# Optimization experiments

Measured on AMD Instinct MI355X. Metric: run time of the kernel, lower is better.

Reference implementation:

```python
import jax, jax.numpy as jnp
import numpy as np

HIDDEN = 2048
FFN = 8192
NUM_EXPERTS = 8
TOP_K = 2


def setup_inputs() -> dict:
    key = jax.random.key(0)
    ks = jax.random.split(key, 6)
    scale_h = 1.0 / np.sqrt(HIDDEN)
    scale_f = 1.0 / np.sqrt(FFN)
    return {
        "hidden_states": jax.random.normal(ks[0], (4, 2048, HIDDEN), jnp.float32),
        "gate_w": jax.random.normal(ks[1], (NUM_EXPERTS, HIDDEN), jnp.float32) * scale_h,
        "w1": jax.random.normal(ks[2], (NUM_EXPERTS, HIDDEN, FFN), jnp.float32) * scale_h,
        "b1": jax.random.normal(ks[3], (NUM_EXPERTS, FFN), jnp.float32) * 0.01,
        "w2": jax.random.normal(ks[4], (NUM_EXPERTS, FFN, HIDDEN), jnp.float32) * scale_f,
        "b2": jax.random.normal(ks[5], (NUM_EXPERTS, HIDDEN), jnp.float32) * 0.01,
    }


def reference(hidden_states, gate_w, w1, b1, w2, b2):
    B, S, H = hidden_states.shape
    E = gate_w.shape[0]
    tokens = hidden_states.reshape(-1, H)  # [T, H]

    # Router: softmax gate, top-2, renormalize selected weights
    logits = tokens @ gate_w.T  # [T, E]
    probs = jax.nn.softmax(logits, axis=-1)
    topk_w, topk_idx = jax.lax.top_k(probs, TOP_K)  # [T, 2]
    topk_w = topk_w / jnp.sum(topk_w, axis=-1, keepdims=True)

    # Dense combine weights: w_dense[t, e] = routing weight of token t for expert e
    w_dense = jnp.sum(jax.nn.one_hot(topk_idx, E, dtype=topk_w.dtype) * topk_w[..., None], axis=1)  # [T, E]

    # Per-expert FFN (exact GELU as nn.GELU default), weighted scatter-combine
    combined = jnp.zeros_like(tokens)
    for e in range(E):  # small fixed expert count
        h = jax.nn.gelu(tokens @ w1[e] + b1[e], approximate=False)  # [T, F]
        combined = combined + w_dense[:, e:e + 1] * (h @ w2[e] + b2[e])

    return combined.reshape(B, S, H) + hidden_states
```

## Files before the change

kernel.cpp:

```cpp
#include <hip/hip_runtime.h>
#include <hip/hip_bf16.h>

#define T_TOK 8192
#define HID 2048
#define FFN_ 8192
#define NE 8
#define MAXR 18432

typedef __attribute__((ext_vector_type(8))) short bf16x8;
typedef __attribute__((ext_vector_type(4))) float f32x4;
typedef __attribute__((ext_vector_type(8))) unsigned short u16x8;

__device__ __forceinline__ unsigned short f2bf(float f) {
  unsigned int u = __float_as_uint(f);
  u += 0x7fffu + ((u >> 16) & 1u);
  return (unsigned short)(u >> 16);
}
__device__ __forceinline__ float bf2f(unsigned short h) {
  return __uint_as_float(((unsigned int)h) << 16);
}

__device__ __forceinline__ void gload_lds16(const ushort* g, ushort* l) {
  __builtin_amdgcn_global_load_lds(
      (const __attribute__((address_space(1))) unsigned int*)g,
      (__attribute__((address_space(3))) unsigned int*)l, 16, 0, 0);
}

__device__ __forceinline__ float gelu_f(float v) {
  float u = v * (0.7978845608f + 0.0356774081f * v * v);
  float a = fabsf(u);
  float ex = __expf(-2.f * a);
  float r = 1.f / (1.f + ex);
  float th = (1.f - ex) * r;
  th = (u >= 0.f) ? th : -th;
  return 0.5f * v * (1.f + th);
}

__global__ __launch_bounds__(256) void router_kernel(
    const float* __restrict__ x, const float* __restrict__ gw,
    int* __restrict__ topk_idx, float* __restrict__ topk_w, int* __restrict__ counts)
{
  int lane = threadIdx.x & 63;
  int w = threadIdx.x >> 6;
  int t = blockIdx.x * 4 + w;
  const float* xr = x + (size_t)t * HID;
  float acc[NE];
#pragma unroll
  for (int e = 0; e < NE; ++e) acc[e] = 0.f;
  for (int h = lane; h < HID; h += 64) {
    float xv = xr[h];
#pragma unroll
    for (int e = 0; e < NE; ++e) acc[e] = fmaf(xv, gw[e * HID + h], acc[e]);
  }
#pragma unroll
  for (int e = 0; e < NE; ++e) {
#pragma unroll
    for (int s = 32; s > 0; s >>= 1) acc[e] += __shfl_xor(acc[e], s);
  }
  if (lane == 0) {
    int i0 = 0; float v0 = acc[0];
#pragma unroll
    for (int e = 1; e < NE; ++e) { if (acc[e] > v0) { v0 = acc[e]; i0 = e; } }
    int i1 = -1; float v1 = -3.4e38f;
#pragma unroll
    for (int e = 0; e < NE; ++e) { if (e != i0 && acc[e] > v1) { v1 = acc[e]; i1 = e; } }
    float r = __expf(v1 - v0);
    float w0 = 1.f / (1.f + r);
    float w1 = r * w0;
    topk_idx[2 * t] = i0; topk_idx[2 * t + 1] = i1;
    topk_w[2 * t] = w0;   topk_w[2 * t + 1] = w1;
    atomicAdd(&counts[i0], 1);
    atomicAdd(&counts[i1], 1);
  }
}

__global__ void offsets_kernel(const int* __restrict__ counts, int* __restrict__ offs) {
  if (threadIdx.x == 0 && blockIdx.x == 0) {
    int o = 0;
#pragma unroll
    for (int e = 0; e < NE; ++e) { offs[e] = o; o += (counts[e] + 255) & ~255; }
    offs[NE] = o;
  }
}

__global__ __launch_bounds__(256) void scatter_kernel(
    const int* __restrict__ topk_idx, const float* __restrict__ topk_w,
    const int* __restrict__ offs, int* __restrict__ cursors,
    int* __restrict__ slot_token, float* __restrict__ slot_w, int* __restrict__ token_slot)
{
  int t = blockIdx.x * blockDim.x + threadIdx.x;
  if (t >= T_TOK) return;
#pragma unroll
  for (int k = 0; k < 2; ++k) {
    int e = topk_idx[2 * t + k];
    int pos = atomicAdd(&cursors[e], 1);
    int slot = offs[e] + pos;
    slot_token[slot] = t;
    slot_w[slot] = topk_w[2 * t + k];
    token_slot[2 * t + k] = slot;
  }
}

__global__ __launch_bounds__(256) void gather_kernel(
    const float* __restrict__ x, const int* __restrict__ slot_token, ushort* __restrict__ Xg)
{
  int row = blockIdx.x;
  int tok = slot_token[row];
  ushort* dst = Xg + (size_t)row * HID + threadIdx.x * 8;
  if (tok < 0) {
    u16x8 z = {0, 0, 0, 0, 0, 0, 0, 0};
    *(u16x8*)dst = z;
  } else {
    const float* s = x + (size_t)tok * HID + threadIdx.x * 8;
    float4 a = *(const float4*)s;
    float4 b = *(const float4*)(s + 4);
    u16x8 v;
    v[0] = f2bf(a.x); v[1] = f2bf(a.y); v[2] = f2bf(a.z); v[3] = f2bf(a.w);
    v[4] = f2bf(b.x); v[5] = f2bf(b.y); v[6] = f2bf(b.z); v[7] = f2bf(b.w);
    *(u16x8*)dst = v;
  }
}

__global__ __launch_bounds__(256) void transpose_convert_kernel(
    const float* __restrict__ src, ushort* __restrict__ dst, int R, int C)
{
  __shared__ float tile[64][65];
  int e = blockIdx.z;
  const float* s = src + (size_t)e * R * C;
  ushort* d = dst + (size_t)e * R * C;
  int r0 = blockIdx.y << 6, c0 = blockIdx.x << 6;
  int t = threadIdx.x;
#pragma unroll
  for (int i = 0; i < 4; ++i) {
    int idx = i * 256 + t;
    int row = idx >> 4;
    int c4 = (idx & 15) << 2;
    float4 v = *(const float4*)&s[(size_t)(r0 + row) * C + (c0 + c4)];
    tile[row][c4 + 0] = v.x; tile[row][c4 + 1] = v.y;
    tile[row][c4 + 2] = v.z; tile[row][c4 + 3] = v.w;
  }
  __syncthreads();
#pragma unroll
  for (int i = 0; i < 8; ++i) {
    int idx = (i * 256 + t) * 2;
    int orow = idx >> 6;
    int ocol = idx & 63;
    ushort2 p;
    p.x = f2bf(tile[ocol][orow]);
    p.y = f2bf(tile[ocol + 1][orow]);
    *(ushort2*)&d[(size_t)(c0 + orow) * R + (r0 + ocol)] = p;
  }
}


#define WAIT_LGKM() do { asm volatile("s_waitcnt lgkmcnt(0)" ::: "memory"); \
                         __builtin_amdgcn_sched_barrier(0); } while (0)
#define WAIT_VM6()  do { asm volatile("s_waitcnt vmcnt(6)" ::: "memory");  \
                         __builtin_amdgcn_sched_barrier(0); } while (0)
#define WAIT_VM0()  do { asm volatile("s_waitcnt vmcnt(0)" ::: "memory");  \
                         __builtin_amdgcn_sched_barrier(0); } while (0)

#define STG_A(BUF, HALF, T) do {                                            \
    ushort* _d = lds + (BUF) * 32768 + (HALF) * 8192 + tid * 8;             \
    gload_lds16(sA0 + (size_t)(HALF) * 64 * K + (size_t)(T) * 64, _d);      \
    gload_lds16(sA1 + (size_t)(HALF) * 64 * K + (size_t)(T) * 64, _d + 4096); \
  } while (0)
#define STG_B(BUF, HALF, T) do {                                            \
    ushort* _d = lds + (BUF) * 32768 + 16384 + (HALF) * 8192 + tid * 8;     \
    gload_lds16(sB0 + (size_t)(HALF) * 32 * K + (size_t)(T) * 64, _d);      \
    gload_lds16(sB1 + (size_t)(HALF) * 32 * K + (size_t)(T) * 64, _d + 4096); \
  } while (0)

#define LDA(BUF, MQ) do {                                                   \
    _Pragma("unroll") for (int mm = 0; mm < 4; ++mm) {                      \
      const ushort* _p = lds + (BUF) * 32768 + (MQ) * 8192 + aoff + mm * 1024; \
      af[mm][0] = *(const bf16x8*)(_p + ck0);                               \
      af[mm][1] = *(const bf16x8*)(_p + ck1);                               \
    } } while (0)
#define LDB(BUF, NQ) do {                                                   \
    _Pragma("unroll") for (int nn = 0; nn < 2; ++nn) {                      \
      const ushort* _p = lds + (BUF) * 32768 + 16384 + (NQ) * 8192 + boff + nn * 1024; \
      bf[NQ][nn][0] = *(const bf16x8*)(_p + ck0);                           \
      bf[NQ][nn][1] = *(const bf16x8*)(_p + ck1);                           \
    } } while (0)

#define MFMA_Q(MQ, NQ) do {                                                 \
    _Pragma("unroll") for (int mm = 0; mm < 4; ++mm)                        \
    _Pragma("unroll") for (int nn = 0; nn < 2; ++nn) {                      \
      acc[(MQ)*4+mm][(NQ)*2+nn] = __builtin_amdgcn_mfma_f32_16x16x32_bf16(  \
          af[mm][0], bf[NQ][nn][0], acc[(MQ)*4+mm][(NQ)*2+nn], 0, 0, 0);    \
      acc[(MQ)*4+mm][(NQ)*2+nn] = __builtin_amdgcn_mfma_f32_16x16x32_bf16(  \
          af[mm][1], bf[NQ][nn][1], acc[(MQ)*4+mm][(NQ)*2+nn], 0, 0, 0);    \
    } } while (0)

#define PH_MFMA(MQ, NQ) do {                                                \
    __builtin_amdgcn_s_barrier();                                           \
    WAIT_LGKM();                                                            \
    __builtin_amdgcn_s_setprio(1);                                          \
    MFMA_Q(MQ, NQ);                                                         \
    __builtin_amdgcn_s_setprio(0);                                          \
    __builtin_amdgcn_sched_barrier(0);                                      \
  } while (0)

template <int EPI>
__global__ __launch_bounds__(512, 2) void gemm256_kernel(
    const ushort* __restrict__ A, const ushort* __restrict__ Bt,
    const float* __restrict__ bias, ushort* __restrict__ Cout,
    const float* __restrict__ slot_w, const int* __restrict__ offs,
    int K, int N, int gy)
{
  __shared__ ushort lds[65536];

  const int tid = threadIdx.x;
  int nwg = gridDim.x;
  int wg = blockIdx.x;
  int cpx = nwg >> 3;
  wg = (wg & 7) * cpx + (wg >> 3);
  int cb = wg / gy;
  int rb = wg - cb * gy;

  int total = offs[NE];
  int row0 = rb * 256;
  if (row0 >= total) return;
  int e = 0;
#pragma unroll
  for (int i = 1; i < NE; ++i) e += (row0 >= offs[i]) ? 1 : 0;

  const ushort* Ag = A + (size_t)row0 * K;
  const ushort* Bg = Bt + ((size_t)e * N + (size_t)cb * 256) * K;

  const int pr0 = tid >> 3;
  const int pr1 = 64 + pr0;
  const int j0 = (tid & 7) ^ (pr0 & 7);
  const int j1 = (tid & 7) ^ (pr1 & 7);
  const int rA0 = pr0;
  const int rA1 = 128 + pr0;
  const int rB0 = ((pr0 >> 5) << 6) + (pr0 & 31);
  const int rB1 = ((pr1 >> 5) << 6) + (pr1 & 31);
  const ushort* sA0 = Ag + (size_t)rA0 * K + j0 * 8;
  const ushort* sA1 = Ag + (size_t)rA1 * K + j1 * 8;
  const ushort* sB0 = Bg + (size_t)rB0 * K + j0 * 8;
  const ushort* sB1 = Bg + (size_t)rB1 * K + j1 * 8;

  const int lane = tid & 63;
  const int wid = tid >> 6;
  const int wr = wid >> 2, wc = wid & 3;
  const int lrow = lane & 15, g = lane >> 4, x7 = lrow & 7;
  const int ck0 = (g ^ x7) * 8;
  const int ck1 = ((4 + g) ^ x7) * 8;
  const int aoff = (wr * 64 + lrow) * 64;
  const int boff = (wc * 32 + lrow) * 64;

  f32x4 acc[8][4] = {};
  bf16x8 af[4][2], bf[2][2][2];

  const int NT = K >> 6;
  const int NITER = NT >> 1;

  STG_A(0, 0, 0); STG_A(0, 1, 0); STG_B(0, 0, 0); STG_B(0, 1, 0);
  STG_A(1, 0, 1); STG_B(1, 0, 1); STG_B(1, 1, 1);
  WAIT_VM6();
  __builtin_amdgcn_s_barrier();

  for (int it = 0; it < NITER; ++it) {
    const int tb = 2 * it + 1;
    const int tn0 = 2 * it + 2;
    const int tn1 = 2 * it + 3;
    const bool more0 = tn0 < NT;
    const bool more1 = tn1 < NT;

    LDA(0, 0); LDB(0, 0);
    STG_A(1, 1, tb);
    PH_MFMA(0, 0);
    __builtin_amdgcn_s_barrier();

    LDB(0, 1);
    if (more0) STG_A(0, 0, tn0);
    PH_MFMA(0, 1);
    __builtin_amdgcn_s_barrier();

    LDA(0, 1);
    if (more0) STG_B(0, 0, tn0);
    PH_MFMA(1, 0);
    __builtin_amdgcn_s_barrier();

    if (more0) STG_B(0, 1, tn0);
    PH_MFMA(1, 1);
    if (it + 1 < NITER) { WAIT_VM6(); } else { WAIT_VM0(); }
    __builtin_amdgcn_s_barrier();

    LDA(1, 0); LDB(1, 0);
    if (more0) STG_A(0, 1, tn0);
    PH_MFMA(0, 0);
    __builtin_amdgcn_s_barrier();

    LDB(1, 1);
    if (more1) STG_A(1, 0, tn1);
    PH_MFMA(0, 1);
    __builtin_amdgcn_s_barrier();

    LDA(1, 1);
    if (more1) STG_B(1, 0, tn1);
    PH_MFMA(1, 0);
    __builtin_amdgcn_s_barrier();

    if (more1) STG_B(1, 1, tn1);
    PH_MFMA(1, 1);
    if (more1) WAIT_VM6();
    __builtin_amdgcn_s_barrier();
  }

  const int colb = cb * 256 + wc * 64;
  const int rowb = row0 + wr * 128;
  float bv[4];
#pragma unroll
  for (int n = 0; n < 4; ++n)
    bv[n] = bias[(size_t)e * N + colb + n * 16 + lrow];
#pragma unroll
  for (int m = 0; m < 8; ++m) {
    const int mq = m >> 2, mm = m & 3;
    const int gr = rowb + mq * 64 + mm * 16 + g * 4;
#pragma unroll
    for (int i = 0; i < 4; ++i) {
      const int grow = gr + i;
      float sw = (EPI == 1) ? slot_w[grow] : 0.f;
      ushort* crow = Cout + (size_t)grow * N + colb + lrow;
#pragma unroll
      for (int n = 0; n < 4; ++n) {
        float v = acc[m][n][i] + bv[n];
        if (EPI == 0) v = gelu_f(v);
        else          v *= sw;
        crow[n * 16] = f2bf(v);
      }
    }
  }
}

__global__ __launch_bounds__(256) void combine_kernel(
    const float* __restrict__ x, const ushort* __restrict__ Yp,
    const int* __restrict__ token_slot, float* __restrict__ out)
{
  int t = blockIdx.x;
  int s0 = token_slot[2 * t], s1 = token_slot[2 * t + 1];
  int c = threadIdx.x * 8;
  const float* xr = x + (size_t)t * HID + c;
  u16x8 y0 = *(const u16x8*)&Yp[(size_t)s0 * HID + c];
  u16x8 y1 = *(const u16x8*)&Yp[(size_t)s1 * HID + c];
  float4 xa = *(const float4*)xr;
  float4 xb = *(const float4*)(xr + 4);
  float4 oa, ob;
  oa.x = xa.x + bf2f(y0[0]) + bf2f(y1[0]);
  oa.y = xa.y + bf2f(y0[1]) + bf2f(y1[1]);
  oa.z = xa.z + bf2f(y0[2]) + bf2f(y1[2]);
  oa.w = xa.w + bf2f(y0[3]) + bf2f(y1[3]);
  ob.x = xb.x + bf2f(y0[4]) + bf2f(y1[4]);
  ob.y = xb.y + bf2f(y0[5]) + bf2f(y1[5]);
  ob.z = xb.z + bf2f(y0[6]) + bf2f(y1[6]);
  ob.w = xb.w + bf2f(y0[7]) + bf2f(y1[7]);
  float* orow = out + (size_t)t * HID + c;
  *(float4*)orow = oa;
  *(float4*)(orow + 4) = ob;
}

extern "C" void kernel_launch(void* const* d_in, const int* in_sizes, int n_in,
                              void* d_out, int out_size, void* d_ws, size_t ws_size,
                              hipStream_t stream)
{
  const float* x  = (const float*)d_in[0];
  const float* gw = (const float*)d_in[1];
  const float* w1 = (const float*)d_in[2];
  const float* b1 = (const float*)d_in[3];
  const float* w2 = (const float*)d_in[4];
  const float* b2 = (const float*)d_in[5];
  float* out = (float*)d_out;

  char* ws = (char*)d_ws;
  ushort* wT  = (ushort*)(ws + 0);
  ushort* Hb  = (ushort*)(ws + 268435456);
  ushort* Xg  = (ushort*)(ws + 570425344);
  ushort* Yp  = Xg;
  char* sm = ws + 645922816;
  int*   slot_token = (int*)(sm);
  float* slot_w     = (float*)(sm + 73728);
  int*   token_slot = (int*)(sm + 147456);
  int*   topk_idx   = (int*)(sm + 212992);
  float* topk_w     = (float*)(sm + 278528);
  int*   counts     = (int*)(sm + 344064);
  int*   cursors    = (int*)(sm + 344096);
  int*   offs       = (int*)(sm + 344128);

  hipMemsetAsync(counts, 0, 64, stream);
  hipMemsetAsync(slot_token, 0xFF, MAXR * 4, stream);

  router_kernel<<<dim3(T_TOK / 4), dim3(256), 0, stream>>>(x, gw, topk_idx, topk_w, counts);
  offsets_kernel<<<dim3(1), dim3(64), 0, stream>>>(counts, offs);
  scatter_kernel<<<dim3(T_TOK / 256), dim3(256), 0, stream>>>(
      topk_idx, topk_w, offs, cursors, slot_token, slot_w, token_slot);
  gather_kernel<<<dim3(MAXR), dim3(256), 0, stream>>>(x, slot_token, Xg);

  transpose_convert_kernel<<<dim3(FFN_ / 64, HID / 64, NE), dim3(256), 0, stream>>>(
      w1, wT, HID, FFN_);
  gemm256_kernel<0><<<dim3((FFN_ / 256) * (MAXR / 256)), dim3(512), 0, stream>>>(
      Xg, wT, b1, Hb, nullptr, offs, HID, FFN_, MAXR / 256);

  transpose_convert_kernel<<<dim3(HID / 64, FFN_ / 64, NE), dim3(256), 0, stream>>>(
      w2, wT, FFN_, HID);
  gemm256_kernel<1><<<dim3((HID / 256) * (MAXR / 256)), dim3(512), 0, stream>>>(
      Hb, wT, b2, Yp, slot_w, offs, FFN_, HID, MAXR / 256);

  combine_kernel<<<dim3(T_TOK), dim3(256), 0, stream>>>(x, Yp, token_slot, out);
}
```

Before: 2.000 ms.

## Reduce per-iteration barriers in GEMM pipeline by regrouping stage loads and MFMA phases

Restructures the double-buffered GEMM main loop so each half-iteration uses one workgroup barrier between pairs of MFMA quadrants, instead of two barriers around every quadrant. Global-to-LDS stage issues are regrouped, with A and B halves of the next tile issued together, and the MFMA phases no longer start with a barrier. This aims to cut synchronisation stalls and let waves drift to overlap LDS reads with MFMA. The trade-off is less lockstep between waves and a risk of LDS read/write hazards if the buffer reuse ordering is subtly wrong.

```diff
diff --git a/kernel.cpp b/kernel.cpp
--- a/kernel.cpp
+++ b/kernel.cpp
@@ -153,12 +153,10 @@
 }
 
 
-#define WAIT_LGKM() do { asm volatile("s_waitcnt lgkmcnt(0)" ::: "memory"); \
-                         __builtin_amdgcn_sched_barrier(0); } while (0)
-#define WAIT_VM6()  do { asm volatile("s_waitcnt vmcnt(6)" ::: "memory");  \
-                         __builtin_amdgcn_sched_barrier(0); } while (0)
-#define WAIT_VM0()  do { asm volatile("s_waitcnt vmcnt(0)" ::: "memory");  \
-                         __builtin_amdgcn_sched_barrier(0); } while (0)
+#define VMW6() do { asm volatile("s_waitcnt vmcnt(6)" ::: "memory"); } while (0)
+#define VMW0() do { asm volatile("s_waitcnt vmcnt(0)" ::: "memory"); } while (0)
+#define SCB()  __builtin_amdgcn_sched_barrier(0)
+#define BAR()  __builtin_amdgcn_s_barrier()
 
 #define STG_A(BUF, HALF, T) do {                                            \
     ushort* _d = lds + (BUF) * 32768 + (HALF) * 8192 + tid * 8;             \
@@ -193,9 +191,9 @@
           af[mm][1], bf[NQ][nn][1], acc[(MQ)*4+mm][(NQ)*2+nn], 0, 0, 0);    \
     } } while (0)
 
-#define PH_MFMA(MQ, NQ) do {                                                \
-    __builtin_amdgcn_s_barrier();                                           \
-    WAIT_LGKM();                                                            \
+#define MM(MQ, NQ) do {                                                     \
+    asm volatile("s_waitcnt lgkmcnt(0)" ::: "memory");                      \
+    __builtin_amdgcn_sched_barrier(0);                                      \
     __builtin_amdgcn_s_setprio(1);                                          \
     MFMA_Q(MQ, NQ);                                                         \
     __builtin_amdgcn_s_setprio(0);                                          \
@@ -259,8 +257,8 @@
 
   STG_A(0, 0, 0); STG_A(0, 1, 0); STG_B(0, 0, 0); STG_B(0, 1, 0);
   STG_A(1, 0, 1); STG_B(1, 0, 1); STG_B(1, 1, 1);
-  WAIT_VM6();
-  __builtin_amdgcn_s_barrier();
+  VMW6();
+  BAR(); SCB();
 
   for (int it = 0; it < NITER; ++it) {
     const int tb = 2 * it + 1;
@@ -268,46 +266,37 @@
     const int tn1 = 2 * it + 3;
     const bool more0 = tn0 < NT;
     const bool more1 = tn1 < NT;
-
+    const bool last = (it + 1 == NITER);
+
+    STG_A(1, 1, tb);
     LDA(0, 0); LDB(0, 0);
-    STG_A(1, 1, tb);
-    PH_MFMA(0, 0);
-    __builtin_amdgcn_s_barrier();
-
+    MM(0, 0);
     LDB(0, 1);
-    if (more0) STG_A(0, 0, tn0);
-    PH_MFMA(0, 1);
-    __builtin_amdgcn_s_barrier();
-
+    MM(0, 1);
+    BAR(); SCB();
+
+    if (more0) { STG_A(0, 0, tn0); STG_B(0, 0, tn0); }
     LDA(0, 1);
-    if (more0) STG_B(0, 0, tn0);
-    PH_MFMA(1, 0);
-    __builtin_amdgcn_s_barrier();
-
+    MM(1, 0);
     if (more0) STG_B(0, 1, tn0);
-    PH_MFMA(1, 1);
-    if (it + 1 < NITER) { WAIT_VM6(); } else { WAIT_VM0(); }
-    __builtin_amdgcn_s_barrier();
-
+    MM(1, 1);
+    if (last) { VMW0(); } else { VMW6(); }
+    BAR(); SCB();
+
+    if (more0) STG_A(0, 1, tn0);
     LDA(1, 0); LDB(1, 0);
-    if (more0) STG_A(0, 1, tn0);
-    PH_MFMA(0, 0);
-    __builtin_amdgcn_s_barrier();
-
+    MM(0, 0);
     LDB(1, 1);
-    if (more1) STG_A(1, 0, tn1);
-    PH_MFMA(0, 1);
-    __builtin_amdgcn_s_barrier();
-
+    MM(0, 1);
+    BAR(); SCB();
+
+    if (more1) { STG_A(1, 0, tn1); STG_B(1, 0, tn1); }
     LDA(1, 1);
-    if (more1) STG_B(1, 0, tn1);
-    PH_MFMA(1, 0);
-    __builtin_amdgcn_s_barrier();
-
+    MM(1, 0);
     if (more1) STG_B(1, 1, tn1);
-    PH_MFMA(1, 1);
-    if (more1) WAIT_VM6();
-    __builtin_amdgcn_s_barrier();
+    MM(1, 1);
+    if (more1) VMW6();
+    BAR(); SCB();
   }
 
   const int colb = cb * 256 + wc * 64;
```

Result: faster. 1.864 ms (-6.8%).
